# Kernel optimization log

Hardware: AMD Instinct MI355X
Metric: run time of the kernel (lower is better)

The kernel has to match this reference:

```python
import jax, jax.numpy as jnp
import numpy as np

HID = 64   # hid_dim // 2 inside pocket_att_net2
H = 8      # n_heads


def _dist_mask(d):
    """get_mask: 8 distance bands, each carrying 1/d inside its band, else 0.
    band i (i=0..6): i < d <= i+3 ; band 7: d > 7.  Output [B, 8, Nl, Np]."""
    safe = jnp.where(d > 0, d, 1.0)
    inv = jnp.where(d > 0, 1.0 / safe, 0.0)
    bands = []
    for i in range(8):
        if i < 7:
            m = (d > float(i)) & (d <= float(i + 3))
        else:
            m = d > 7.0
        bands.append(jnp.where(m, inv, 0.0))
    return jnp.stack(bands, axis=1)


def setup_inputs() -> dict:
    key = jax.random.key(0)
    ks = jax.random.split(key, 20)
    B, Nl, Np = 16, 256, 2048
    s = 0.05
    inp = {
        "ligand": jax.random.normal(ks[0], (B, Nl, HID), jnp.float32),
        "prot":   jax.random.normal(ks[1], (B, Np, HID), jnp.float32),
        "dist":   jax.random.uniform(ks[2], (B, Nl, Np), jnp.float32) * 10.0,
        # projection weights (jax convention: x @ W + b)
        "w_l1": jax.random.normal(ks[3], (HID, HID * H), jnp.float32) * s,
        "b_l1": jnp.zeros((HID * H,), jnp.float32),
        "w_l2": jax.random.normal(ks[4], (HID, HID * H), jnp.float32) * s,
        "b_l2": jnp.zeros((HID * H,), jnp.float32),
        "w_p1": jax.random.normal(ks[5], (HID, HID * H), jnp.float32) * s,
        "b_p1": jnp.zeros((HID * H,), jnp.float32),
        "w_p2": jax.random.normal(ks[6], (HID, HID * H), jnp.float32) * s,
        "b_p2": jnp.zeros((HID * H,), jnp.float32),
        "fc11_w": jax.random.normal(ks[7], (HID * H, HID), jnp.float32) * s,
        "fc11_b": jnp.zeros((HID,), jnp.float32),
        "fc12_w": jax.random.normal(ks[8], (2 * HID, HID), jnp.float32) * s,
        "fc12_b": jnp.zeros((HID,), jnp.float32),
        "fc21_w": jax.random.normal(ks[9], (HID * H, HID), jnp.float32) * s,
        "fc21_b": jnp.zeros((HID,), jnp.float32),
        "fc22_w": jax.random.normal(ks[10], (2 * HID, HID), jnp.float32) * s,
        "fc22_b": jnp.zeros((HID,), jnp.float32),
    }
    return inp


def _proj(x, w, b):
    B, N, _ = x.shape
    h = jax.nn.relu(x @ w + b)                      # [B, N, H*HID]
    return h.reshape(B, N, H, HID).transpose(0, 2, 1, 3)  # [B, H, N, HID]


def reference(ligand, prot, dist, w_l1, b_l1, w_l2, b_l2, w_p1, b_p1, w_p2, b_p2,
              fc11_w, fc11_b, fc12_w, fc12_b, fc21_w, fc21_b, fc22_w, fc22_b):
    B, Nl, _ = ligand.shape
    Np = prot.shape[1]
    inter = _dist_mask(dist)                        # [B, H, Nl, Np]

    l1 = _proj(ligand, w_l1, b_l1)
    l2 = _proj(ligand, w_l2, b_l2)
    p1 = _proj(prot, w_p1, b_p1)
    p2 = _proj(prot, w_p2, b_p2)

    scale = jnp.sqrt(jnp.float32(HID))
    energy = jnp.einsum('bhld,bhpd->bhlp', l1, p1) / scale
    att = jax.nn.softmax(energy * inter, axis=-1)   # dropout = identity (eval)

    l3 = jnp.einsum('bhlp,bhpd->bhld', att, p2)
    l3 = l3.transpose(0, 2, 1, 3).reshape(B, Nl, H * HID)
    l3 = jnp.concatenate([l3 @ fc11_w + fc11_b, ligand], axis=2)
    l3 = jax.nn.relu(l3 @ fc12_w + fc12_b)          # [B, Nl, HID]

    p3 = jnp.einsum('bhlp,bhld->bhpd', att, l2)
    p3 = p3.transpose(0, 2, 1, 3).reshape(B, Np, H * HID)
    p3 = jnp.concatenate([p3 @ fc21_w + fc21_b, prot], axis=2)
    p3 = jax.nn.relu(p3 @ fc22_w + fc22_b)          # [B, Np, HID]

    return jnp.concatenate([l3, p3], axis=1)        # [B, Nl+Np, HID]
```

## Files before the change

### kernel.cpp

```cpp
#include <hip/hip_runtime.h>
#include <hip/hip_bf16.h>

typedef _Float16 f16x8 __attribute__((ext_vector_type(8)));
typedef _Float16 f16x4 __attribute__((ext_vector_type(4)));
typedef float f32x4 __attribute__((ext_vector_type(4)));

#define B_   16
#define NL   256
#define NP   2048
#define NH   8
#define PSPLIT 4
#define PCHUNK (NP / PSPLIT)

static __device__ __forceinline__ f32x4 mfma16(f16x8 a, f16x8 b, f32x4 c) {
  return __builtin_amdgcn_mfma_f32_16x16x32_f16(a, b, c, 0, 0, 0);
}

__global__ __launch_bounds__(256) void proj_kernel(
    const float* __restrict__ x, const float* __restrict__ W, const float* __restrict__ bias,
    _Float16* __restrict__ outA, _Float16* __restrict__ outB, int N, int mode)
{
  __shared__ float xt[64][68];
  const int t = threadIdx.x;
  const int n0 = blockIdx.x * 64;
  const int h  = blockIdx.y;
  const int b  = blockIdx.z;

  const float* xp = x + ((size_t)b * N + n0) * 64;
#pragma unroll
  for (int i = 0; i < 4; ++i) {
    int flat = (i * 256 + t) * 4;
    f32x4 v = *(const f32x4*)(xp + flat);
    *(f32x4*)&xt[flat >> 6][flat & 63] = v;
  }
  __syncthreads();

  const int nb = (t >> 4) * 4;
  const int db = (t & 15) * 4;

  float acc[4][4];
#pragma unroll
  for (int i = 0; i < 4; ++i)
#pragma unroll
    for (int j = 0; j < 4; ++j) acc[i][j] = bias[h * 64 + db + j];

  const float* wp = W + h * 64 + db;
#pragma unroll 8
  for (int k = 0; k < 64; ++k) {
    f32x4 wq = *(const f32x4*)(wp + (size_t)k * 512);
    float a0 = xt[nb + 0][k], a1 = xt[nb + 1][k], a2 = xt[nb + 2][k], a3 = xt[nb + 3][k];
#pragma unroll
    for (int j = 0; j < 4; ++j) {
      acc[0][j] += a0 * wq[j];
      acc[1][j] += a1 * wq[j];
      acc[2][j] += a2 * wq[j];
      acc[3][j] += a3 * wq[j];
    }
  }

  if (mode == 0) {
#pragma unroll
    for (int i = 0; i < 4; ++i) {
      f16x4 hv, lv;
#pragma unroll
      for (int j = 0; j < 4; ++j) {
        float v = fmaxf(acc[i][j], 0.f);
        _Float16 hi = (_Float16)v;
        hv[j] = hi;
        lv[j] = (_Float16)((v - (float)hi) * 2048.0f);
      }
      size_t idx = (((size_t)b * NH + h) * N + n0 + nb + i) * 64 + db;
      *(f16x4*)(outA + idx) = hv;
      *(f16x4*)(outB + idx) = lv;
    }
  } else {
#pragma unroll
    for (int j = 0; j < 4; ++j) {
      f16x4 tv;
#pragma unroll
      for (int i = 0; i < 4; ++i) tv[i] = (_Float16)fmaxf(acc[i][j], 0.f);
      size_t idx = (((size_t)b * NH + h) * 64 + db + j) * N + n0 + nb;
      *(f16x4*)(outA + idx) = tv;
    }
  }
}

__global__ __launch_bounds__(512) void flash_l3_kernel(
    const _Float16* __restrict__ l1h, const _Float16* __restrict__ l1l,
    const _Float16* __restrict__ p1h, const _Float16* __restrict__ p1l,
    const _Float16* __restrict__ p2t, const float* __restrict__ dist,
    float* __restrict__ l3p, float* __restrict__ mpart, float* __restrict__ spart)
{
  const int sb = blockIdx.x;
  const int sp = sb & (PSPLIT - 1);
  const int b  = sb >> 2;
  const int lt = blockIdx.y;
  const int t  = threadIdx.x;
  const int h    = t >> 6;
  const int lane = t & 63;
  const int g = lane >> 4, c = lane & 15;
  const int l0 = lt * 16;
  const int bh = b * NH + h;

  __shared__ _Float16 P[NH][16][72];

  const size_t l1off = ((size_t)bh * NL + l0 + c) * 64;
  f16x8 aLh[2], aLl[2];
  aLh[0] = *(const f16x8*)(l1h + l1off + g * 8);
  aLh[1] = *(const f16x8*)(l1h + l1off + 32 + g * 8);
  aLl[0] = *(const f16x8*)(l1l + l1off + g * 8);
  aLl[1] = *(const f16x8*)(l1l + l1off + 32 + g * 8);

  f32x4 accO[4];
#pragma unroll
  for (int dt = 0; dt < 4; ++dt) accO[dt] = (f32x4){0.f, 0.f, 0.f, 0.f};
  float m_r[4] = {-INFINITY, -INFINITY, -INFINITY, -INFINITY};
  float s_r[4] = {0.f, 0.f, 0.f, 0.f};

  const float* dbase = dist + ((size_t)b * NL + l0) * NP + sp * PCHUNK;
  const _Float16* p1hb = p1h + ((size_t)bh * NP + sp * PCHUNK) * 64;
  const _Float16* p1lb = p1l + ((size_t)bh * NP + sp * PCHUNK) * 64;
  const _Float16* p2tb = p2t + (size_t)bh * 64 * NP + sp * PCHUNK;
  const float fh = (float)h, fh3 = fh + 3.0f;

  for (int P0 = 0; P0 < PCHUNK; P0 += 64) {
    float mev[4][4];
    float cmax[4] = {-INFINITY, -INFINITY, -INFINITY, -INFINITY};
#pragma unroll
    for (int s = 0; s < 4; ++s) {
      const _Float16* ph = p1hb + (size_t)(P0 + s * 16 + c) * 64;
      const _Float16* pl = p1lb + (size_t)(P0 + s * 16 + c) * 64;
      f16x8 bh0 = *(const f16x8*)(ph + g * 8);
      f16x8 bh1 = *(const f16x8*)(ph + 32 + g * 8);
      f16x8 bl0 = *(const f16x8*)(pl + g * 8);
      f16x8 bl1 = *(const f16x8*)(pl + 32 + g * 8);
      const float* drow = dbase + P0 + s * 16 + c;
      float d0 = drow[(size_t)(g * 4 + 0) * NP];
      float d1 = drow[(size_t)(g * 4 + 1) * NP];
      float d2 = drow[(size_t)(g * 4 + 2) * NP];
      float d3 = drow[(size_t)(g * 4 + 3) * NP];
      f32x4 e  = (f32x4){0.f, 0.f, 0.f, 0.f};
      f32x4 ec = (f32x4){0.f, 0.f, 0.f, 0.f};
      e  = mfma16(aLh[0], bh0, e);  e  = mfma16(aLh[1], bh1, e);
      ec = mfma16(aLh[0], bl0, ec); ec = mfma16(aLh[1], bl1, ec);
      ec = mfma16(aLl[0], bh0, ec); ec = mfma16(aLl[1], bh1, ec);
      f32x4 dq = (f32x4){d0, d1, d2, d3};
#pragma unroll
      for (int r = 0; r < 4; ++r) {
        float dv = dq[r];
        float ev = (e[r] + ec[r] * (1.0f / 2048.0f)) * 0.125f;
        bool cond = (h < 7) ? (dv > fh && dv <= fh3) : (dv > 7.0f);
        float m = cond ? ev * __builtin_amdgcn_rcpf(dv) : 0.0f;
        mev[s][r] = m;
        cmax[r] = fmaxf(cmax[r], m);
      }
    }
#pragma unroll
    for (int mask = 1; mask < 16; mask <<= 1)
#pragma unroll
      for (int r = 0; r < 4; ++r)
        cmax[r] = fmaxf(cmax[r], __shfl_xor(cmax[r], mask, 64));

#pragma unroll
    for (int r = 0; r < 4; ++r) {
      float mn  = fmaxf(m_r[r], cmax[r]);
      float fac = __expf(m_r[r] - mn);
      m_r[r] = mn;
      float ss = 0.f;
#pragma unroll
      for (int s = 0; s < 4; ++s) {
        float pv = __expf(mev[s][r] - mn);
        ss += pv;
        P[h][g * 4 + r][s * 16 + c] = (_Float16)pv;
      }
      s_r[r] = s_r[r] * fac + ss;
#pragma unroll
      for (int dt = 0; dt < 4; ++dt) accO[dt][r] *= fac;
    }
#pragma unroll
    for (int kk = 0; kk < 2; ++kk) {
      f16x8 aP = *(const f16x8*)&P[h][c][kk * 32 + g * 8];
#pragma unroll
      for (int dt = 0; dt < 4; ++dt) {
        f16x8 bV = *(const f16x8*)(p2tb + (size_t)(dt * 16 + c) * NP + P0 + kk * 32 + g * 8);
        accO[dt] = mfma16(aP, bV, accO[dt]);
      }
    }
  }

#pragma unroll
  for (int mask = 1; mask < 16; mask <<= 1)
#pragma unroll
    for (int r = 0; r < 4; ++r) s_r[r] += __shfl_xor(s_r[r], mask, 64);

  float* lp = l3p + (size_t)sp * B_ * NL * 512;
#pragma unroll
  for (int dt = 0; dt < 4; ++dt)
#pragma unroll
    for (int r = 0; r < 4; ++r)
      lp[((size_t)b * NL + l0 + g * 4 + r) * 512 + h * 64 + dt * 16 + c] = accO[dt][r];

  if (c == 0) {
#pragma unroll
    for (int r = 0; r < 4; ++r) {
      size_t li = (size_t)sp * B_ * NH * NL + (size_t)bh * NL + l0 + g * 4 + r;
      mpart[li] = m_r[r];
      spart[li] = s_r[r];
    }
  }
}

__global__ __launch_bounds__(256) void merge_l3_kernel(
    const float* __restrict__ l3p, const float* __restrict__ mpart, const float* __restrict__ spart,
    float* __restrict__ l3c, float* __restrict__ mrow, float* __restrict__ rsrow)
{
  const int row = blockIdx.x * 4 + (threadIdx.x >> 6);
  const int d   = threadIdx.x & 63;
  const int l   = row & (NL - 1);
  const int bh  = row >> 8;
  const int b = bh >> 3, h = bh & 7;
  const size_t srow = (size_t)B_ * NH * NL;

  float mi[PSPLIT], si[PSPLIT];
  float M = -INFINITY;
#pragma unroll
  for (int i = 0; i < PSPLIT; ++i) {
    mi[i] = mpart[(size_t)i * srow + row];
    si[i] = spart[(size_t)i * srow + row];
    M = fmaxf(M, mi[i]);
  }
  const float* lp = l3p + ((size_t)b * NL + l) * 512 + h * 64 + d;
  float S = 0.f, o = 0.f;
#pragma unroll
  for (int i = 0; i < PSPLIT; ++i) {
    float w = __expf(mi[i] - M);
    S += si[i] * w;
    o += lp[(size_t)i * B_ * NL * 512] * w;
  }
  float rs = 1.0f / S;
  l3c[((size_t)b * NL + l) * 512 + h * 64 + d] = o * rs;
  if (d == 0) { mrow[row] = M; rsrow[row] = rs; }
}

__global__ __launch_bounds__(512) void p3_kernel(
    const _Float16* __restrict__ p1h, const _Float16* __restrict__ p1l,
    const _Float16* __restrict__ l1h, const _Float16* __restrict__ l1l,
    const _Float16* __restrict__ l2t, const float* __restrict__ dist,
    const float* __restrict__ mrow, const float* __restrict__ rsrow,
    float* __restrict__ p3c)
{
  const int b  = blockIdx.x;
  const int pt = blockIdx.y;
  const int t  = threadIdx.x;
  const int h    = t >> 6;
  const int lane = t & 63;
  const int g = lane >> 4, c = lane & 15;
  const int p0 = pt * 16;
  const int bh = b * NH + h;

  __shared__ _Float16 PT[NH][16][40];

  const size_t poff = ((size_t)bh * NP + p0 + c) * 64;
  f16x8 aPh[2], aPl[2];
  aPh[0] = *(const f16x8*)(p1h + poff + g * 8);
  aPh[1] = *(const f16x8*)(p1h + poff + 32 + g * 8);
  aPl[0] = *(const f16x8*)(p1l + poff + g * 8);
  aPl[1] = *(const f16x8*)(p1l + poff + 32 + g * 8);

  f32x4 acc[4];
#pragma unroll
  for (int dt = 0; dt < 4; ++dt) acc[dt] = (f32x4){0.f, 0.f, 0.f, 0.f};

  const float* db_ = dist + (size_t)b * NL * NP + p0;
  const _Float16* l1hb = l1h + (size_t)bh * NL * 64;
  const _Float16* l1lb = l1l + (size_t)bh * NL * 64;
  const _Float16* l2tb = l2t + (size_t)bh * 64 * NL;
  const float* mb = mrow + (size_t)bh * NL;
  const float* rb = rsrow + (size_t)bh * NL;
  const float fh = (float)h, fh3 = fh + 3.0f;

  for (int lc = 0; lc < NL; lc += 32) {
#pragma unroll
    for (int s = 0; s < 2; ++s) {
      const int l = lc + s * 16 + c;
      const _Float16* lhp = l1hb + (size_t)l * 64;
      const _Float16* llp = l1lb + (size_t)l * 64;
      f16x8 bh0 = *(const f16x8*)(lhp + g * 8);
      f16x8 bh1 = *(const f16x8*)(lhp + 32 + g * 8);
      f16x8 bl0 = *(const f16x8*)(llp + g * 8);
      f16x8 bl1 = *(const f16x8*)(llp + 32 + g * 8);
      f32x4 e  = (f32x4){0.f, 0.f, 0.f, 0.f};
      f32x4 ec = (f32x4){0.f, 0.f, 0.f, 0.f};
      e  = mfma16(aPh[0], bh0, e);  e  = mfma16(aPh[1], bh1, e);
      ec = mfma16(aPh[0], bl0, ec); ec = mfma16(aPh[1], bl1, ec);
      ec = mfma16(aPl[0], bh0, ec); ec = mfma16(aPl[1], bh1, ec);
      float ml = mb[l], rl = rb[l];
      f32x4 dq = *(const f32x4*)(db_ + (size_t)l * NP + g * 4);
#pragma unroll
      for (int r = 0; r < 4; ++r) {
        float ev = (e[r] + ec[r] * (1.0f / 2048.0f)) * 0.125f;
        float dvv = dq[r];
        bool cond = (h < 7) ? (dvv > fh && dvv <= fh3) : (dvv > 7.0f);
        float m = cond ? ev * __builtin_amdgcn_rcpf(dvv) : 0.0f;
        float att = __expf(m - ml) * rl;
        PT[h][g * 4 + r][s * 16 + c] = (_Float16)att;
      }
    }
    {
      f16x8 aA = *(const f16x8*)&PT[h][c][g * 8];
#pragma unroll
      for (int dt = 0; dt < 4; ++dt) {
        f16x8 bV = *(const f16x8*)(l2tb + (size_t)(dt * 16 + c) * NL + lc + g * 8);
        acc[dt] = mfma16(aA, bV, acc[dt]);
      }
    }
  }

#pragma unroll
  for (int dt = 0; dt < 4; ++dt)
#pragma unroll
    for (int r = 0; r < 4; ++r)
      p3c[((size_t)b * NP + p0 + g * 4 + r) * 512 + h * 64 + dt * 16 + c] = acc[dt][r];
}

__global__ __launch_bounds__(256) void fc_out_kernel(
    const float* __restrict__ x3c, const float* __restrict__ xbase,
    const float* __restrict__ wA, const float* __restrict__ bA,
    const float* __restrict__ wB, const float* __restrict__ bB,
    float* __restrict__ out, int N, int out_off)
{
  __shared__ float xl[16][520];
  __shared__ float t1[16][68];
  __shared__ float xb[16][68];
  const int t = threadIdx.x;
  const int row0 = blockIdx.x * 16;

  const float* xp = x3c + (size_t)row0 * 512;
#pragma unroll
  for (int i = 0; i < 8; ++i) {
    int flat = (i * 256 + t) * 4;
    f32x4 v = *(const f32x4*)(xp + flat);
    *(f32x4*)&xl[flat >> 9][flat & 511] = v;
  }
  {
    const float* bp = xbase + (size_t)row0 * 64;
    int flat = t * 4;
    f32x4 v = *(const f32x4*)(bp + flat);
    *(f32x4*)&xb[flat >> 6][flat & 63] = v;
  }
  __syncthreads();

  const int r  = t >> 4;
  const int c4 = (t & 15) * 4;

  float acc[4];
#pragma unroll
  for (int j = 0; j < 4; ++j) acc[j] = bA[c4 + j];
  for (int k4 = 0; k4 < 128; ++k4) {
    f32x4 xq = *(const f32x4*)&xl[r][k4 * 4];
#pragma unroll
    for (int kk = 0; kk < 4; ++kk) {
      f32x4 wq = *(const f32x4*)(wA + (size_t)(k4 * 4 + kk) * 64 + c4);
#pragma unroll
      for (int j = 0; j < 4; ++j) acc[j] += xq[kk] * wq[j];
    }
  }
#pragma unroll
  for (int j = 0; j < 4; ++j) t1[r][c4 + j] = acc[j];
  __syncthreads();

  float a2[4];
#pragma unroll
  for (int j = 0; j < 4; ++j) a2[j] = bB[c4 + j];
  for (int k4 = 0; k4 < 32; ++k4) {
    f32x4 xq = (k4 < 16) ? *(const f32x4*)&t1[r][k4 * 4]
                         : *(const f32x4*)&xb[r][k4 * 4 - 64];
#pragma unroll
    for (int kk = 0; kk < 4; ++kk) {
      f32x4 wq = *(const f32x4*)(wB + (size_t)(k4 * 4 + kk) * 64 + c4);
#pragma unroll
      for (int j = 0; j < 4; ++j) a2[j] += xq[kk] * wq[j];
    }
  }
  const int row = row0 + r;
  const int b = row / N, n = row % N;
  f32x4 o;
#pragma unroll
  for (int j = 0; j < 4; ++j) o[j] = fmaxf(a2[j], 0.f);
  *(f32x4*)(out + (((size_t)b * (NL + NP)) + out_off + n) * 64 + c4) = o;
}

extern "C" void kernel_launch(void* const* d_in, const int* in_sizes, int n_in,
                              void* d_out, int out_size, void* d_ws, size_t ws_size,
                              hipStream_t stream)
{
  const float* ligand = (const float*)d_in[0];
  const float* prot   = (const float*)d_in[1];
  const float* dist   = (const float*)d_in[2];
  const float* w_l1   = (const float*)d_in[3];
  const float* b_l1   = (const float*)d_in[4];
  const float* w_l2   = (const float*)d_in[5];
  const float* b_l2   = (const float*)d_in[6];
  const float* w_p1   = (const float*)d_in[7];
  const float* b_p1   = (const float*)d_in[8];
  const float* w_p2   = (const float*)d_in[9];
  const float* b_p2   = (const float*)d_in[10];
  const float* fc11_w = (const float*)d_in[11];
  const float* fc11_b = (const float*)d_in[12];
  const float* fc12_w = (const float*)d_in[13];
  const float* fc12_b = (const float*)d_in[14];
  const float* fc21_w = (const float*)d_in[15];
  const float* fc21_b = (const float*)d_in[16];
  const float* fc22_w = (const float*)d_in[17];
  const float* fc22_b = (const float*)d_in[18];
  float* out = (float*)d_out;

  char* ws = (char*)d_ws;
  size_t off = 0;
  auto alloc = [&](size_t bytes) -> void* {
    void* p = ws + off;
    off += (bytes + 255) & ~(size_t)255;
    return p;
  };
  const size_t L1E = (size_t)B_ * NH * NL * 64;
  const size_t P1E = (size_t)B_ * NH * NP * 64;
  _Float16* l1h = (_Float16*)alloc(L1E * 2);
  _Float16* l1l = (_Float16*)alloc(L1E * 2);
  _Float16* p1h = (_Float16*)alloc(P1E * 2);
  _Float16* p1l = (_Float16*)alloc(P1E * 2);
  _Float16* l2t = (_Float16*)alloc(L1E * 2);
  _Float16* p2t = (_Float16*)alloc(P1E * 2);
  float* mrow  = (float*)alloc((size_t)B_ * NH * NL * 4);
  float* rsrow = (float*)alloc((size_t)B_ * NH * NL * 4);
  float* mpart = (float*)alloc((size_t)PSPLIT * B_ * NH * NL * 4);
  float* spart = (float*)alloc((size_t)PSPLIT * B_ * NH * NL * 4);
  float* l3c = (float*)alloc((size_t)B_ * NL * 512 * 4);
  float* p3c = (float*)alloc((size_t)B_ * NP * 512 * 4);
  float* l3p = p3c;

  proj_kernel<<<dim3(NL / 64, NH, B_), 256, 0, stream>>>(ligand, w_l1, b_l1, l1h, l1l, NL, 0);
  proj_kernel<<<dim3(NL / 64, NH, B_), 256, 0, stream>>>(ligand, w_l2, b_l2, l2t, nullptr, NL, 1);
  proj_kernel<<<dim3(NP / 64, NH, B_), 256, 0, stream>>>(prot, w_p1, b_p1, p1h, p1l, NP, 0);
  proj_kernel<<<dim3(NP / 64, NH, B_), 256, 0, stream>>>(prot, w_p2, b_p2, p2t, nullptr, NP, 1);

  flash_l3_kernel<<<dim3(PSPLIT * B_, NL / 16), 512, 0, stream>>>(
      l1h, l1l, p1h, p1l, p2t, dist, l3p, mpart, spart);
  merge_l3_kernel<<<(B_ * NH * NL) / 4, 256, 0, stream>>>(l3p, mpart, spart, l3c, mrow, rsrow);
  p3_kernel<<<dim3(B_, NP / 16), 512, 0, stream>>>(p1h, p1l, l1h, l1l, l2t, dist,
                                                   mrow, rsrow, p3c);

  fc_out_kernel<<<(B_ * NL) / 16, 256, 0, stream>>>(l3c, ligand, fc11_w, fc11_b,
                                                    fc12_w, fc12_b, out, NL, 0);
  fc_out_kernel<<<(B_ * NP) / 16, 256, 0, stream>>>(p3c, prot, fc21_w, fc21_b,
                                                    fc22_w, fc22_b, out, NP, NL);
}
```

Baseline: 840.4 us.

## Stage distance tiles in shared memory with double-buffered prefetch in both attention kernels

Both the flash_l3 and p3 kernels now load each distance tile cooperatively into a double-buffered shared-memory buffer, prefetching the next tile into registers while the current one is used. Previously every wave loaded all distance values separately with strided global reads, and those loads were duplicated across the 8 heads. The p2/l2 value operands are also loaded at the top of each iteration so they are in flight during the energy MFMAs. The MFMA sections are wrapped in s_setprio, and launch bounds now request 4 blocks per CU. The cost is an added __syncthreads per tile and more register pressure from the hoisted loads.

```diff
diff --git a/kernel.cpp b/kernel.cpp
--- a/kernel.cpp
+++ b/kernel.cpp
@@ -85,7 +85,7 @@
   }
 }
 
-__global__ __launch_bounds__(512) void flash_l3_kernel(
+__global__ __launch_bounds__(512, 4) void flash_l3_kernel(
     const _Float16* __restrict__ l1h, const _Float16* __restrict__ l1l,
     const _Float16* __restrict__ p1h, const _Float16* __restrict__ p1l,
     const _Float16* __restrict__ p2t, const float* __restrict__ dist,
@@ -101,7 +101,9 @@
   const int g = lane >> 4, c = lane & 15;
   const int l0 = lt * 16;
   const int bh = b * NH + h;
-
+  const int NT = PCHUNK / 64;
+
+  __shared__ float distT[2][64][20];
   __shared__ _Float16 P[NH][16][72];
 
   const size_t l1off = ((size_t)bh * NL + l0 + c) * 64;
@@ -123,7 +125,35 @@
   const _Float16* p2tb = p2t + (size_t)bh * 64 * NP + sp * PCHUNK;
   const float fh = (float)h, fh3 = fh + 3.0f;
 
-  for (int P0 = 0; P0 < PCHUNK; P0 += 64) {
+  const int dl_p = t & 63;
+  const int dl_l = t >> 6;
+
+  {
+    float dv0 = dbase[(size_t)dl_l * NP + dl_p];
+    float dv1 = dbase[(size_t)(dl_l + 8) * NP + dl_p];
+    distT[0][dl_p][dl_l]     = dv0;
+    distT[0][dl_p][dl_l + 8] = dv1;
+  }
+
+  for (int it = 0; it < NT; ++it) {
+    const int P0 = it * 64;
+    const int cur = it & 1;
+    __syncthreads();
+
+    float nv0 = 0.f, nv1 = 0.f;
+    if (it + 1 < NT) {
+      nv0 = dbase[(size_t)dl_l * NP + P0 + 64 + dl_p];
+      nv1 = dbase[(size_t)(dl_l + 8) * NP + P0 + 64 + dl_p];
+    }
+
+    f16x8 v0[4], v1[4];
+#pragma unroll
+    for (int dt = 0; dt < 4; ++dt) {
+      const _Float16* vp = p2tb + (size_t)(dt * 16 + c) * NP + P0 + g * 8;
+      v0[dt] = *(const f16x8*)(vp);
+      v1[dt] = *(const f16x8*)(vp + 32);
+    }
+
     float mev[4][4];
     float cmax[4] = {-INFINITY, -INFINITY, -INFINITY, -INFINITY};
 #pragma unroll
@@ -134,17 +164,14 @@
       f16x8 bh1 = *(const f16x8*)(ph + 32 + g * 8);
       f16x8 bl0 = *(const f16x8*)(pl + g * 8);
       f16x8 bl1 = *(const f16x8*)(pl + 32 + g * 8);
-      const float* drow = dbase + P0 + s * 16 + c;
-      float d0 = drow[(size_t)(g * 4 + 0) * NP];
-      float d1 = drow[(size_t)(g * 4 + 1) * NP];
-      float d2 = drow[(size_t)(g * 4 + 2) * NP];
-      float d3 = drow[(size_t)(g * 4 + 3) * NP];
       f32x4 e  = (f32x4){0.f, 0.f, 0.f, 0.f};
       f32x4 ec = (f32x4){0.f, 0.f, 0.f, 0.f};
+      __builtin_amdgcn_s_setprio(1);
       e  = mfma16(aLh[0], bh0, e);  e  = mfma16(aLh[1], bh1, e);
       ec = mfma16(aLh[0], bl0, ec); ec = mfma16(aLh[1], bl1, ec);
       ec = mfma16(aLl[0], bh0, ec); ec = mfma16(aLl[1], bh1, ec);
-      f32x4 dq = (f32x4){d0, d1, d2, d3};
+      __builtin_amdgcn_s_setprio(0);
+      f32x4 dq = *(const f32x4*)&distT[cur][s * 16 + c][g * 4];
 #pragma unroll
       for (int r = 0; r < 4; ++r) {
         float dv = dq[r];
@@ -177,14 +204,19 @@
 #pragma unroll
       for (int dt = 0; dt < 4; ++dt) accO[dt][r] *= fac;
     }
-#pragma unroll
-    for (int kk = 0; kk < 2; ++kk) {
-      f16x8 aP = *(const f16x8*)&P[h][c][kk * 32 + g * 8];
-#pragma unroll
-      for (int dt = 0; dt < 4; ++dt) {
-        f16x8 bV = *(const f16x8*)(p2tb + (size_t)(dt * 16 + c) * NP + P0 + kk * 32 + g * 8);
-        accO[dt] = mfma16(aP, bV, accO[dt]);
-      }
+    {
+      f16x8 aP0 = *(const f16x8*)&P[h][c][g * 8];
+      f16x8 aP1 = *(const f16x8*)&P[h][c][32 + g * 8];
+      __builtin_amdgcn_s_setprio(1);
+#pragma unroll
+      for (int dt = 0; dt < 4; ++dt) accO[dt] = mfma16(aP0, v0[dt], accO[dt]);
+#pragma unroll
+      for (int dt = 0; dt < 4; ++dt) accO[dt] = mfma16(aP1, v1[dt], accO[dt]);
+      __builtin_amdgcn_s_setprio(0);
+    }
+    if (it + 1 < NT) {
+      distT[cur ^ 1][dl_p][dl_l]     = nv0;
+      distT[cur ^ 1][dl_p][dl_l + 8] = nv1;
     }
   }
 
@@ -242,7 +274,7 @@
   if (d == 0) { mrow[row] = M; rsrow[row] = rs; }
 }
 
-__global__ __launch_bounds__(512) void p3_kernel(
+__global__ __launch_bounds__(512, 4) void p3_kernel(
     const _Float16* __restrict__ p1h, const _Float16* __restrict__ p1l,
     const _Float16* __restrict__ l1h, const _Float16* __restrict__ l1l,
     const _Float16* __restrict__ l2t, const float* __restrict__ dist,
@@ -257,7 +289,9 @@
   const int g = lane >> 4, c = lane & 15;
   const int p0 = pt * 16;
   const int bh = b * NH + h;
-
+  const int NT = NL / 32;
+
+  __shared__ float distT[2][32][20];
   __shared__ _Float16 PT[NH][16][40];
 
   const size_t poff = ((size_t)bh * NP + p0 + c) * 64;
@@ -279,7 +313,25 @@
   const float* rb = rsrow + (size_t)bh * NL;
   const float fh = (float)h, fh3 = fh + 3.0f;
 
-  for (int lc = 0; lc < NL; lc += 32) {
+  const int dl_l = t >> 4;
+  const int dl_p = t & 15;
+
+  distT[0][dl_l][dl_p] = db_[(size_t)dl_l * NP + dl_p];
+
+  for (int it = 0; it < NT; ++it) {
+    const int lc = it * 32;
+    const int cur = it & 1;
+    __syncthreads();
+
+    float nv = 0.f;
+    if (it + 1 < NT)
+      nv = db_[(size_t)(lc + 32 + dl_l) * NP + dl_p];
+
+    f16x8 bV[4];
+#pragma unroll
+    for (int dt = 0; dt < 4; ++dt)
+      bV[dt] = *(const f16x8*)(l2tb + (size_t)(dt * 16 + c) * NL + lc + g * 8);
+
 #pragma unroll
     for (int s = 0; s < 2; ++s) {
       const int l = lc + s * 16 + c;
@@ -291,11 +343,13 @@
       f16x8 bl1 = *(const f16x8*)(llp + 32 + g * 8);
       f32x4 e  = (f32x4){0.f, 0.f, 0.f, 0.f};
       f32x4 ec = (f32x4){0.f, 0.f, 0.f, 0.f};
+      __builtin_amdgcn_s_setprio(1);
       e  = mfma16(aPh[0], bh0, e);  e  = mfma16(aPh[1], bh1, e);
       ec = mfma16(aPh[0], bl0, ec); ec = mfma16(aPh[1], bl1, ec);
       ec = mfma16(aPl[0], bh0, ec); ec = mfma16(aPl[1], bh1, ec);
+      __builtin_amdgcn_s_setprio(0);
       float ml = mb[l], rl = rb[l];
-      f32x4 dq = *(const f32x4*)(db_ + (size_t)l * NP + g * 4);
+      f32x4 dq = *(const f32x4*)&distT[cur][s * 16 + c][g * 4];
 #pragma unroll
       for (int r = 0; r < 4; ++r) {
         float ev = (e[r] + ec[r] * (1.0f / 2048.0f)) * 0.125f;
@@ -308,12 +362,13 @@
     }
     {
       f16x8 aA = *(const f16x8*)&PT[h][c][g * 8];
-#pragma unroll
-      for (int dt = 0; dt < 4; ++dt) {
-        f16x8 bV = *(const f16x8*)(l2tb + (size_t)(dt * 16 + c) * NL + lc + g * 8);
-        acc[dt] = mfma16(aA, bV, acc[dt]);
-      }
-    }
+      __builtin_amdgcn_s_setprio(1);
+#pragma unroll
+      for (int dt = 0; dt < 4; ++dt) acc[dt] = mfma16(aA, bV[dt], acc[dt]);
+      __builtin_amdgcn_s_setprio(0);
+    }
+    if (it + 1 < NT)
+      distT[cur ^ 1][dl_l][dl_p] = nv;
   }
 
 #pragma unroll
```

Measured after the change: 870.5 us. 3.6% more time.
